# Optimization experiments

Measured on AMD Instinct MI355X. Metric: run time of the kernel, lower is better.

The kernel has to match this reference:

```python
import jax, jax.numpy as jnp
import numpy as np

B, L, D = 2, 2048, 1024
H, HD = 16, 64
MAX_LEN = 4096


def rotate_half(t):
    t1, t2 = jnp.split(t, 2, axis=-1)
    return jnp.concatenate([-t2, t1], axis=-1)


def setup_inputs() -> dict:
    key = jax.random.key(0)
    ks = jax.random.split(key, 6)
    # rope tables computed the standard way (cos/sin of position*inv_freq)
    inv_freq = 1.0 / (10000.0 ** (np.arange(0, HD, 2, dtype=np.float32) / HD))
    pos = np.arange(MAX_LEN, dtype=np.float32)
    freqs = np.einsum('l,f->lf', pos, inv_freq)          # [MAX_LEN, HD/2]
    emb = np.concatenate([freqs, freqs], axis=-1)        # [MAX_LEN, HD]
    return {
        'x': jax.random.normal(ks[0], (B, L, D), dtype=jnp.float32),
        'rope_cos': jnp.asarray(np.cos(emb)),
        'rope_sin': jnp.asarray(np.sin(emb)),
        'W_qkv': jax.random.normal(ks[1], (D, 3 * H * HD), dtype=jnp.float32) * (D ** -0.5),
        'W_out': jax.random.normal(ks[2], (H * HD, D), dtype=jnp.float32) * ((H * HD) ** -0.5),
        'b_out': jnp.zeros((D,), dtype=jnp.float32),
    }


def reference(x, rope_cos, rope_sin, W_qkv, W_out, b_out):
    Bb, Ll, Dd = x.shape
    qkv = jnp.einsum('bld,de->ble', x, W_qkv)            # fused QKV projection
    q, k, v = jnp.split(qkv, 3, axis=-1)
    # [B, h, L, d]
    q = q.reshape(Bb, Ll, H, HD).transpose(0, 2, 1, 3)
    k = k.reshape(Bb, Ll, H, HD).transpose(0, 2, 1, 3)
    v = v.reshape(Bb, Ll, H, HD).transpose(0, 2, 1, 3)
    cos = rope_cos[:Ll][None, None, :, :]                # [1,1,L,d]
    sin = rope_sin[:Ll][None, None, :, :]
    q = q * cos + rotate_half(q) * sin
    k = k * cos + rotate_half(k) * sin
    # causal scaled dot-product attention
    scale = HD ** -0.5
    scores = jnp.einsum('bhqd,bhkd->bhqk', q, k) * scale
    causal = jnp.tril(jnp.ones((Ll, Ll), dtype=bool))
    scores = jnp.where(causal[None, None], scores, jnp.finfo(scores.dtype).min)
    attn = jax.nn.softmax(scores, axis=-1)
    out = jnp.einsum('bhqk,bhkd->bhqd', attn, v)
    out = out.transpose(0, 2, 1, 3).reshape(Bb, Ll, H * HD)
    return jnp.einsum('ble,ed->bld', out, W_out) + b_out
```

## Files before the change

kernel.cpp:

```cpp
#include <hip/hip_runtime.h>
#include <math.h>

#define BQ 2
#define LQ 2048
#define DQ 1024
#define HQ 16
#define HDQ 64

typedef __bf16 bf16_t;
typedef bf16_t bf16x4 __attribute__((ext_vector_type(4)));
typedef bf16_t bf16x8 __attribute__((ext_vector_type(8)));
typedef _Float16 f16_t;
typedef f16_t f16x4 __attribute__((ext_vector_type(4)));
typedef f16_t f16x8 __attribute__((ext_vector_type(8)));
typedef float f32x4 __attribute__((ext_vector_type(4)));

__global__ __launch_bounds__(256) void prep_kernel(
    const float* __restrict__ x, const float* __restrict__ Wqkv,
    const float* __restrict__ Wout, const float* __restrict__ cosT,
    const float* __restrict__ sinT,
    bf16_t* __restrict__ xb, bf16_t* __restrict__ Wqkvt,
    bf16_t* __restrict__ Wot, float4* __restrict__ rpk)
{
    __shared__ float t[32][33];
    const int bid = blockIdx.x, tid = threadIdx.x;
    if (bid < 4096) {
        const int i = (bid * 256 + tid) * 4;
        float4 v = *(const float4*)(x + i);
        bf16x4 o;
        o[0] = (bf16_t)v.x; o[1] = (bf16_t)v.y; o[2] = (bf16_t)v.z; o[3] = (bf16_t)v.w;
        *(bf16x4*)(xb + i) = o;
    } else if (bid < 8192) {
        const bool isq = bid < 7168;
        const int b = isq ? bid - 4096 : bid - 7168;
        const int N = isq ? 3072 : 1024;
        const int gx = isq ? 96 : 32;
        const float* in = isq ? Wqkv : Wout;
        bf16_t* out = isq ? Wqkvt : Wot;
        const int k0 = (b / gx) * 32, n0 = (b % gx) * 32;
        const int r = tid >> 3, c4 = (tid & 7) * 4;
        float4 v = *(const float4*)(in + (size_t)(k0 + r) * N + n0 + c4);
        t[r][c4 + 0] = v.x; t[r][c4 + 1] = v.y;
        t[r][c4 + 2] = v.z; t[r][c4 + 3] = v.w;
        __syncthreads();
        bf16x4 o;
        o[0] = (bf16_t)t[c4 + 0][r]; o[1] = (bf16_t)t[c4 + 1][r];
        o[2] = (bf16_t)t[c4 + 2][r]; o[3] = (bf16_t)t[c4 + 3][r];
        *(bf16x4*)(out + (size_t)(n0 + r) * 1024 + k0 + c4) = o;
    } else {
        const int idx = (bid - 8192) * 256 + tid;
        const int i = idx & 15, l = idx >> 4;
        rpk[idx] = make_float4(cosT[l * 64 + i], cosT[l * 64 + 16 + i],
                               sinT[l * 64 + i], sinT[l * 64 + 16 + i]);
    }
}

__global__ __launch_bounds__(256) void qkv_gemm_kernel(
    const bf16_t* __restrict__ A, const bf16_t* __restrict__ Bt,
    bf16_t* __restrict__ qo, bf16_t* __restrict__ ko, f16_t* __restrict__ vo,
    const float4* __restrict__ rpk)
{
    __shared__ __align__(16) bf16_t As[2][128][32];
    __shared__ __align__(16) bf16_t Bs[2][128][32];
    const int K = 1024;
    const int tid  = threadIdx.x;
    const int lane = tid & 63;
    const int w    = tid >> 6;
    const int lr   = lane & 15, quad = lane >> 4;
    const int wm   = w & 1, wn = w >> 1;
    const int m0   = blockIdx.y * 128, n0 = blockIdx.x * 128;

    const int sr  = tid >> 2;
    const int sc  = tid & 3;
    const int sw  = (sc ^ ((sr >> 1) & 3)) * 8;
    const int rdc = (quad ^ ((lr >> 1) & 3)) * 8;

    const bf16_t* Ar0 = A  + (size_t)(m0 + sr) * K + sc * 8;
    const bf16_t* Ar1 = A  + (size_t)(m0 + sr + 64) * K + sc * 8;
    const bf16_t* Br0 = Bt + (size_t)(n0 + sr) * K + sc * 8;
    const bf16_t* Br1 = Bt + (size_t)(n0 + sr + 64) * K + sc * 8;

    f32x4 acc[4][4];
#pragma unroll
    for (int i = 0; i < 4; i++)
#pragma unroll
        for (int j = 0; j < 4; j++)
#pragma unroll
            for (int r = 0; r < 4; r++) acc[i][j][r] = 0.f;

#define QLOAD(A0, A1, B0, B1, t) do {                      \
        A0 = *(const bf16x8*)(Ar0 + (t) * 32);             \
        A1 = *(const bf16x8*)(Ar1 + (t) * 32);             \
        B0 = *(const bf16x8*)(Br0 + (t) * 32);             \
        B1 = *(const bf16x8*)(Br1 + (t) * 32);             \
    } while (0)
#define QWRITE(A0, A1, B0, B1, bf) do {                    \
        *(bf16x8*)(&As[bf][sr][sw])      = A0;             \
        *(bf16x8*)(&As[bf][sr + 64][sw]) = A1;             \
        *(bf16x8*)(&Bs[bf][sr][sw])      = B0;             \
        *(bf16x8*)(&Bs[bf][sr + 64][sw]) = B1;             \
    } while (0)
#define QCOMP(bf) do {                                                        \
        bf16x8 af[4], bfr[4];                                                 \
        _Pragma("unroll")                                                     \
        for (int tt = 0; tt < 4; tt++) {                                      \
            af[tt]  = *(const bf16x8*)(&As[bf][wm * 64 + tt * 16 + lr][rdc]); \
            bfr[tt] = *(const bf16x8*)(&Bs[bf][wn * 64 + tt * 16 + lr][rdc]); \
        }                                                                     \
        _Pragma("unroll")                                                     \
        for (int mt = 0; mt < 4; mt++)                                        \
            _Pragma("unroll")                                                 \
            for (int nt = 0; nt < 4; nt++)                                    \
                acc[mt][nt] = __builtin_amdgcn_mfma_f32_16x16x32_bf16(        \
                    af[mt], bfr[nt], acc[mt][nt], 0, 0, 0);                   \
    } while (0)

    bf16x8 a00, a10, b00, b10;
    bf16x8 a01, a11, b01, b11;
    QLOAD(a00, a10, b00, b10, 0);
    QLOAD(a01, a11, b01, b11, 1);
    QWRITE(a00, a10, b00, b10, 0);
    __syncthreads();

    for (int t = 0; t < 32; t += 2) {
        if (t + 2 < 32) QLOAD(a00, a10, b00, b10, t + 2);
        QCOMP(0);
        QWRITE(a01, a11, b01, b11, 1);
        __syncthreads();
        if (t + 3 < 32) QLOAD(a01, a11, b01, b11, t + 3);
        QCOMP(1);
        if (t + 2 < 32) QWRITE(a00, a10, b00, b10, 0);
        __syncthreads();
    }
#undef QLOAD
#undef QWRITE
#undef QCOMP

    const int which = n0 >> 10;
    const int h = ((n0 & 1023) + wn * 64) >> 6;
    if (which == 2) {
#pragma unroll
        for (int mt = 0; mt < 4; mt++) {
            const int m = m0 + wm * 64 + mt * 16 + quad * 4;
            const int b = m >> 11, l = m & 2047;
            f16_t* p = vo + ((size_t)(b * HQ + h) * HDQ) * LQ + l;
#pragma unroll
            for (int nt = 0; nt < 4; nt++) {
                f16x4 pv;
#pragma unroll
                for (int r = 0; r < 4; r++) pv[r] = (f16_t)acc[mt][nt][r];
                *(f16x4*)(p + (size_t)(nt * 16 + lr) * LQ) = pv;
            }
        }
    } else {
        bf16_t* dst = which ? ko : qo;
        const float qs = which ? 1.0f : 0.18033688011f;
#pragma unroll
        for (int mt = 0; mt < 4; mt++)
#pragma unroll
            for (int r = 0; r < 4; r++) {
                const int m = m0 + wm * 64 + mt * 16 + quad * 4 + r;
                const int b = m >> 11, l = m & 2047;
                const float4 rp = rpk[l * 16 + lr];
                const float a0 = acc[mt][0][r], a1 = acc[mt][1][r];
                const float a2 = acc[mt][2][r], a3 = acc[mt][3][r];
                bf16_t* p = dst + ((size_t)(b * HQ + h) * LQ + l) * HDQ;
                p[lr]      = (bf16_t)((a0 * rp.x - a2 * rp.z) * qs);
                p[16 + lr] = (bf16_t)((a1 * rp.y - a3 * rp.w) * qs);
                p[32 + lr] = (bf16_t)((a2 * rp.x + a0 * rp.z) * qs);
                p[48 + lr] = (bf16_t)((a3 * rp.y + a1 * rp.w) * qs);
            }
    }
}

__global__ __launch_bounds__(256) void out_gemm_kernel(
    const bf16_t* __restrict__ A, const bf16_t* __restrict__ Bt,
    float* __restrict__ fo, const float* __restrict__ bias)
{
    __shared__ __align__(16) bf16_t As[64][64];
    __shared__ __align__(16) bf16_t Bs[128][64];
    const int K = 1024, N = 1024;
    const int tid  = threadIdx.x;
    const int lane = tid & 63;
    const int w    = tid >> 6;
    const int lr   = lane & 15, quad = lane >> 4;
    const int m0   = blockIdx.y * 64, n0 = blockIdx.x * 128;
    const int srow8 = lane >> 3;
    const int swz   = ((lane & 7) ^ srow8) * 8;
    const int wc    = (lane & 7) * 8;

    f32x4 acc[4][2];
#pragma unroll
    for (int i = 0; i < 4; i++)
#pragma unroll
        for (int j = 0; j < 2; j++)
#pragma unroll
            for (int r = 0; r < 4; r++) acc[i][j][r] = 0.f;

    bf16x8 ar[2], br[4];
#pragma unroll
    for (int j = 0; j < 2; j++)
        ar[j] = *(const bf16x8*)(A + (size_t)(m0 + (w * 2 + j) * 8 + srow8) * K + swz);
#pragma unroll
    for (int j = 0; j < 4; j++)
        br[j] = *(const bf16x8*)(Bt + (size_t)(n0 + (w * 4 + j) * 8 + srow8) * K + swz);

    for (int k0 = 0; k0 < K; k0 += 64) {
        __syncthreads();
#pragma unroll
        for (int j = 0; j < 2; j++)
            *(bf16x8*)(&As[(w * 2 + j) * 8 + srow8][wc]) = ar[j];
#pragma unroll
        for (int j = 0; j < 4; j++)
            *(bf16x8*)(&Bs[(w * 4 + j) * 8 + srow8][wc]) = br[j];
        __syncthreads();
        if (k0 + 64 < K) {
#pragma unroll
            for (int j = 0; j < 2; j++)
                ar[j] = *(const bf16x8*)(A + (size_t)(m0 + (w * 2 + j) * 8 + srow8) * K
                                          + k0 + 64 + swz);
#pragma unroll
            for (int j = 0; j < 4; j++)
                br[j] = *(const bf16x8*)(Bt + (size_t)(n0 + (w * 4 + j) * 8 + srow8) * K
                                          + k0 + 64 + swz);
        }

        bf16x8 af[4][2], bfr[2][2];
#pragma unroll
        for (int h = 0; h < 2; h++) {
            const int cA = ((quad + 4 * h) ^ (lr & 7)) * 8;
#pragma unroll
            for (int t = 0; t < 4; t++)
                af[t][h] = *(const bf16x8*)(&As[t * 16 + lr][cA]);
#pragma unroll
            for (int t = 0; t < 2; t++)
                bfr[t][h] = *(const bf16x8*)(&Bs[w * 32 + t * 16 + lr][cA]);
        }
#pragma unroll
        for (int h = 0; h < 2; h++)
#pragma unroll
            for (int mt = 0; mt < 4; mt++)
#pragma unroll
                for (int nt = 0; nt < 2; nt++)
                    acc[mt][nt] = __builtin_amdgcn_mfma_f32_16x16x32_bf16(
                        af[mt][h], bfr[nt][h], acc[mt][nt], 0, 0, 0);
    }

#pragma unroll
    for (int nt = 0; nt < 2; nt++) {
        const int n = n0 + w * 32 + nt * 16 + lr;
        const float bj = bias[n];
#pragma unroll
        for (int mt = 0; mt < 4; mt++)
#pragma unroll
            for (int r = 0; r < 4; r++) {
                const int m = m0 + mt * 16 + quad * 4 + r;
                fo[(size_t)m * N + n] = acc[mt][nt][r] + bj;
            }
    }
}

__global__ __launch_bounds__(512) void attn_kernel10(
    const bf16_t* __restrict__ qb, const bf16_t* __restrict__ kb,
    const f16_t* __restrict__ vtb, bf16_t* __restrict__ ob)
{
    __shared__ __align__(16) bf16_t Kb[2][64][64];
    __shared__ __align__(16) f16_t  Vs[2][64][68];

    const int tid  = threadIdx.x;
    const int lane = tid & 63;
    const int w    = tid >> 6;
    const int quad = lane >> 4;
    const int lr   = lane & 15;
    const int bh   = blockIdx.x;
    const int qt2  = 15 - blockIdx.y;

    const bf16_t* Kh = kb  + (size_t)bh * LQ * HDQ;
    const f16_t*  Vh = vtb + (size_t)bh * HDQ * LQ;

    const int r0  = tid >> 3;
    const int c0  = (tid & 7) * 8;
    const int ksw = ((tid & 7) ^ (r0 & 7)) * 8;

    f16x4 ones;
#pragma unroll
    for (int j = 0; j < 4; j++) ones[j] = (f16_t)1.0f;

    const int qbase = qt2 * 128 + w * 16;
    const int qrow  = qbase + lr;
    const bf16_t* qp = qb + ((size_t)bh * LQ + qrow) * HDQ;
    const bf16x8 qa0 = *(const bf16x8*)(qp + quad * 8);
    const bf16x8 qa1 = *(const bf16x8*)(qp + 32 + quad * 8);

    const int nkt = 2 * qt2 + 2;

    bf16x8 kp = *(const bf16x8*)(Kh + (size_t)r0 * HDQ + c0);
    f16x8  vp = *(const f16x8*)(Vh + (size_t)r0 * LQ + c0);

    f32x4 Oacc[4], lacc;
#pragma unroll
    for (int d = 0; d < 4; d++)
#pragma unroll
        for (int r = 0; r < 4; r++) Oacc[d][r] = 0.f;
#pragma unroll
    for (int r = 0; r < 4; r++) lacc[r] = 0.f;

    for (int kt = 0; kt < nkt; kt++) {
        const int buf = kt & 1;
        *(bf16x8*)(&Kb[buf][r0][ksw]) = kp;
        *(f16x8*)(&Vs[buf][r0][c0]) = vp;
        __syncthreads();
        if (kt + 1 < nkt) {
            kp = *(const bf16x8*)(Kh + (size_t)((kt + 1) * 64 + r0) * HDQ + c0);
            vp = *(const f16x8*)(Vh + (size_t)r0 * LQ + (kt + 1) * 64 + c0);
        }

        if (kt * 64 <= qbase + 15) {
            f32x4 s[4];
            __builtin_amdgcn_s_setprio(1);
#pragma unroll
            for (int nt = 0; nt < 4; nt++) {
                const int rsw = lr & 7;
                const bf16x8 kf0 = *(const bf16x8*)(&Kb[buf][nt * 16 + lr][(quad ^ rsw) * 8]);
                const bf16x8 kf1 = *(const bf16x8*)(&Kb[buf][nt * 16 + lr][((quad + 4) ^ rsw) * 8]);
                f32x4 z = {0.f, 0.f, 0.f, 0.f};
                z = __builtin_amdgcn_mfma_f32_16x16x32_bf16(kf0, qa0, z, 0, 0, 0);
                z = __builtin_amdgcn_mfma_f32_16x16x32_bf16(kf1, qa1, z, 0, 0, 0);
                s[nt] = z;
            }
            __builtin_amdgcn_s_setprio(0);
            if (kt * 64 + 63 > qbase) {
#pragma unroll
                for (int nt = 0; nt < 4; nt++)
#pragma unroll
                    for (int r = 0; r < 4; r++)
                        if (kt * 64 + nt * 16 + quad * 4 + r > qrow) s[nt][r] = -INFINITY;
            }
            f16x4 pa[4];
#pragma unroll
            for (int nt = 0; nt < 4; nt++)
#pragma unroll
                for (int r = 0; r < 4; r++)
                    pa[nt][r] = (f16_t)__builtin_amdgcn_exp2f(s[nt][r]);

            __builtin_amdgcn_s_setprio(1);
#pragma unroll
            for (int d = 0; d < 4; d++)
#pragma unroll
                for (int nt = 0; nt < 4; nt++) {
                    const f16x4 vf = *(const f16x4*)(&Vs[buf][d * 16 + lr][nt * 16 + quad * 4]);
                    Oacc[d] = __builtin_amdgcn_mfma_f32_16x16x16f16(pa[nt], vf, Oacc[d], 0, 0, 0);
                }
#pragma unroll
            for (int nt = 0; nt < 4; nt++)
                lacc = __builtin_amdgcn_mfma_f32_16x16x16f16(pa[nt], ones, lacc, 0, 0, 0);
            __builtin_amdgcn_s_setprio(0);
        }
    }

    const int b = bh >> 4, h = bh & 15;
#pragma unroll
    for (int r = 0; r < 4; r++) {
        const float inv = 1.0f / lacc[r];
        const int q = qbase + quad * 4 + r;
        bf16_t* op = ob + ((size_t)(b * LQ + q)) * 1024 + h * 64;
#pragma unroll
        for (int d = 0; d < 4; d++)
            op[d * 16 + lr] = (bf16_t)(Oacc[d][r] * inv);
    }
}

extern "C" void kernel_launch(void* const* d_in, const int* in_sizes, int n_in,
                              void* d_out, int out_size, void* d_ws, size_t ws_size,
                              hipStream_t stream) {
    const float* x        = (const float*)d_in[0];
    const float* rope_cos = (const float*)d_in[1];
    const float* rope_sin = (const float*)d_in[2];
    const float* W_qkv    = (const float*)d_in[3];
    const float* W_out    = (const float*)d_in[4];
    const float* b_out    = (const float*)d_in[5];
    float* out = (float*)d_out;

    char* wsb = (char*)d_ws;
    bf16_t* xb    = (bf16_t*)(wsb);
    bf16_t* qbf   = (bf16_t*)(wsb + ((size_t)8  << 20));
    bf16_t* kbf   = (bf16_t*)(wsb + ((size_t)16 << 20));
    f16_t*  vth   = (f16_t*) (wsb + ((size_t)24 << 20));
    bf16_t* ob    = (bf16_t*)(wsb + ((size_t)32 << 20));
    bf16_t* Wqkvt = (bf16_t*)(wsb + ((size_t)40 << 20));
    bf16_t* Wot   = (bf16_t*)(wsb + ((size_t)46 << 20));
    float4* rpk   = (float4*)(wsb + ((size_t)48 << 20));

    prep_kernel<<<8320, 256, 0, stream>>>(x, W_qkv, W_out, rope_cos, rope_sin,
                                          xb, Wqkvt, Wot, rpk);

    dim3 g1(3072 / 128, 4096 / 128);
    qkv_gemm_kernel<<<g1, 256, 0, stream>>>(xb, Wqkvt, qbf, kbf, vth, rpk);

    dim3 g2(32, 16);
    attn_kernel10<<<g2, 512, 0, stream>>>(qbf, kbf, vth, ob);

    dim3 g3(1024 / 128, 4096 / 64);
    out_gemm_kernel<<<g3, 256, 0, stream>>>(ob, Wot, out, b_out);
}
```

Before: 174.6 us.

## Double-buffer out-projection GEMM LDS tiles with 32-wide K steps and two-deep prefetch

Result: no change. 174.5 us (-0.1%).

```diff
diff --git a/kernel.cpp b/kernel.cpp
--- a/kernel.cpp
+++ b/kernel.cpp
@@ -177,17 +177,23 @@
     const bf16_t* __restrict__ A, const bf16_t* __restrict__ Bt,
     float* __restrict__ fo, const float* __restrict__ bias)
 {
-    __shared__ __align__(16) bf16_t As[64][64];
-    __shared__ __align__(16) bf16_t Bs[128][64];
+    __shared__ __align__(16) bf16_t As[2][64][32];
+    __shared__ __align__(16) bf16_t Bs[2][128][32];
     const int K = 1024, N = 1024;
     const int tid  = threadIdx.x;
     const int lane = tid & 63;
     const int w    = tid >> 6;
     const int lr   = lane & 15, quad = lane >> 4;
     const int m0   = blockIdx.y * 64, n0 = blockIdx.x * 128;
-    const int srow8 = lane >> 3;
-    const int swz   = ((lane & 7) ^ srow8) * 8;
-    const int wc    = (lane & 7) * 8;
+
+    const int sr  = tid >> 2;
+    const int sc  = tid & 3;
+    const int sw  = (sc ^ ((sr >> 1) & 3)) * 8;
+    const int rdc = (quad ^ ((lr >> 1) & 3)) * 8;
+
+    const bf16_t* Ar0 = A  + (size_t)(m0 + sr) * K + sc * 8;
+    const bf16_t* Br0 = Bt + (size_t)(n0 + sr) * K + sc * 8;
+    const bf16_t* Br1 = Bt + (size_t)(n0 + sr + 64) * K + sc * 8;
 
     f32x4 acc[4][2];
 #pragma unroll
@@ -197,54 +203,52 @@
 #pragma unroll
             for (int r = 0; r < 4; r++) acc[i][j][r] = 0.f;
 
-    bf16x8 ar[2], br[4];
-#pragma unroll
-    for (int j = 0; j < 2; j++)
-        ar[j] = *(const bf16x8*)(A + (size_t)(m0 + (w * 2 + j) * 8 + srow8) * K + swz);
-#pragma unroll
-    for (int j = 0; j < 4; j++)
-        br[j] = *(const bf16x8*)(Bt + (size_t)(n0 + (w * 4 + j) * 8 + srow8) * K + swz);
-
-    for (int k0 = 0; k0 < K; k0 += 64) {
-        __syncthreads();
-#pragma unroll
-        for (int j = 0; j < 2; j++)
-            *(bf16x8*)(&As[(w * 2 + j) * 8 + srow8][wc]) = ar[j];
-#pragma unroll
-        for (int j = 0; j < 4; j++)
-            *(bf16x8*)(&Bs[(w * 4 + j) * 8 + srow8][wc]) = br[j];
-        __syncthreads();
-        if (k0 + 64 < K) {
-#pragma unroll
-            for (int j = 0; j < 2; j++)
-                ar[j] = *(const bf16x8*)(A + (size_t)(m0 + (w * 2 + j) * 8 + srow8) * K
-                                          + k0 + 64 + swz);
-#pragma unroll
-            for (int j = 0; j < 4; j++)
-                br[j] = *(const bf16x8*)(Bt + (size_t)(n0 + (w * 4 + j) * 8 + srow8) * K
-                                          + k0 + 64 + swz);
-        }
-
-        bf16x8 af[4][2], bfr[2][2];
-#pragma unroll
-        for (int h = 0; h < 2; h++) {
-            const int cA = ((quad + 4 * h) ^ (lr & 7)) * 8;
-#pragma unroll
-            for (int t = 0; t < 4; t++)
-                af[t][h] = *(const bf16x8*)(&As[t * 16 + lr][cA]);
-#pragma unroll
-            for (int t = 0; t < 2; t++)
-                bfr[t][h] = *(const bf16x8*)(&Bs[w * 32 + t * 16 + lr][cA]);
-        }
-#pragma unroll
-        for (int h = 0; h < 2; h++)
-#pragma unroll
-            for (int mt = 0; mt < 4; mt++)
-#pragma unroll
-                for (int nt = 0; nt < 2; nt++)
-                    acc[mt][nt] = __builtin_amdgcn_mfma_f32_16x16x32_bf16(
-                        af[mt][h], bfr[nt][h], acc[mt][nt], 0, 0, 0);
-    }
+#define OLOAD(A0, B0, B1, t) do {                          \
+        A0 = *(const bf16x8*)(Ar0 + (t) * 32);             \
+        B0 = *(const bf16x8*)(Br0 + (t) * 32);             \
+        B1 = *(const bf16x8*)(Br1 + (t) * 32);             \
+    } while (0)
+#define OWRITE(A0, B0, B1, bf) do {                        \
+        *(bf16x8*)(&As[bf][sr][sw])      = A0;             \
+        *(bf16x8*)(&Bs[bf][sr][sw])      = B0;             \
+        *(bf16x8*)(&Bs[bf][sr + 64][sw]) = B1;             \
+    } while (0)
+#define OCOMP(bf) do {                                                        \
+        bf16x8 af[4], bfr[2];                                                 \
+        _Pragma("unroll")                                                     \
+        for (int tt = 0; tt < 4; tt++)                                        \
+            af[tt]  = *(const bf16x8*)(&As[bf][tt * 16 + lr][rdc]);           \
+        _Pragma("unroll")                                                     \
+        for (int tt = 0; tt < 2; tt++)                                        \
+            bfr[tt] = *(const bf16x8*)(&Bs[bf][w * 32 + tt * 16 + lr][rdc]);  \
+        _Pragma("unroll")                                                     \
+        for (int mt = 0; mt < 4; mt++)                                        \
+            _Pragma("unroll")                                                 \
+            for (int nt = 0; nt < 2; nt++)                                    \
+                acc[mt][nt] = __builtin_amdgcn_mfma_f32_16x16x32_bf16(        \
+                    af[mt], bfr[nt], acc[mt][nt], 0, 0, 0);                   \
+    } while (0)
+
+    bf16x8 a0s0, b0s0, b1s0;
+    bf16x8 a0s1, b0s1, b1s1;
+    OLOAD(a0s0, b0s0, b1s0, 0);
+    OLOAD(a0s1, b0s1, b1s1, 1);
+    OWRITE(a0s0, b0s0, b1s0, 0);
+    __syncthreads();
+
+    for (int t = 0; t < 32; t += 2) {
+        if (t + 2 < 32) OLOAD(a0s0, b0s0, b1s0, t + 2);
+        OCOMP(0);
+        OWRITE(a0s1, b0s1, b1s1, 1);
+        __syncthreads();
+        if (t + 3 < 32) OLOAD(a0s1, b0s1, b1s1, t + 3);
+        OCOMP(1);
+        if (t + 2 < 32) OWRITE(a0s0, b0s0, b1s0, 0);
+        __syncthreads();
+    }
+#undef OLOAD
+#undef OWRITE
+#undef OCOMP
 
 #pragma unroll
     for (int nt = 0; nt < 2; nt++) {
```
